# Kernel optimization log

Measured on AMD Instinct MI355X. Metric: run time of the kernel, lower is better.

Reference implementation:

```python
import jax, jax.numpy as jnp
import numpy as np

N = 50000        # nodes
E = 1_600_000    # edges (avg degree 32)
IN = 8           # in_channels
OUT = 64         # out_channels / hidden
K = 2            # Chebyshev order


def setup_inputs() -> dict:
    key = jax.random.key(0)
    ks = jax.random.split(key, 16)
    w = lambda k, s: (jax.random.normal(k, s, jnp.float32) * 0.05)
    inp = {
        "x": jax.random.normal(ks[0], (N, IN), jnp.float32),
        "H": jax.random.normal(ks[1], (N, OUT), jnp.float32),
        "edge_index": jax.random.randint(ks[2], (2, E), 0, N, dtype=jnp.int64),
    }
    names = [("z_x", IN), ("z_h", OUT), ("r_x", IN), ("r_h", OUT), ("c_x", IN), ("c_h", OUT)]
    for i, (nm, d) in enumerate(names):
        inp["W_" + nm] = w(ks[3 + 2 * i], (K, d, OUT))
        inp["b_" + nm] = w(ks[4 + 2 * i], (OUT,))
    return inp


def _cheb(x, W, b, row, col, norm):
    # PyG-style ChebConv with lambda_max=2: L_hat = -D^{-1/2} A D^{-1/2}
    # Tx0 = x; Tx1 = L_hat x; Tx_k = 2 L_hat Tx_{k-1} - Tx_{k-2}
    out = x @ W[0]
    Tx0 = x
    Tx1 = jax.ops.segment_sum(norm[:, None] * x[col], row, num_segments=N)
    out = out + Tx1 @ W[1]
    for k in range(2, W.shape[0]):
        Tx2 = 2.0 * jax.ops.segment_sum(norm[:, None] * Tx1[col], row, num_segments=N) - Tx0
        out = out + Tx2 @ W[k]
        Tx0, Tx1 = Tx1, Tx2
    return out + b


def reference(x, H, edge_index, W_z_x, b_z_x, W_z_h, b_z_h, W_r_x, b_r_x,
              W_r_h, b_r_h, W_c_x, b_c_x, W_c_h, b_c_h):
    row, col = edge_index[0], edge_index[1]
    deg = jax.ops.segment_sum(jnp.ones((E,), x.dtype), row, num_segments=N)
    dinv = jnp.where(deg > 0, 1.0 / jnp.sqrt(jnp.where(deg > 0, deg, 1.0)), 0.0)
    norm = -dinv[row] * dinv[col]  # sym-normalized, negated adjacency (L - I)

    Z = jax.nn.sigmoid(_cheb(x, W_z_x, b_z_x, row, col, norm)
                       + _cheb(H, W_z_h, b_z_h, row, col, norm))
    R = jax.nn.sigmoid(_cheb(x, W_r_x, b_r_x, row, col, norm)
                       + _cheb(H, W_r_h, b_r_h, row, col, norm))
    C = jnp.tanh(_cheb(x, W_c_x, b_c_x, row, col, norm)
                 + _cheb(R * H, W_c_h, b_c_h, row, col, norm))
    return Z * H + (1.0 - Z) * C
```

## Files before the change

### kernel.cpp

```cpp
#include <hip/hip_runtime.h>
#include <math.h>

#define IN_CH 8
#define OUT_CH 64

__global__ void deg_kernel(const int* __restrict__ row, int* __restrict__ deg, int E) {
    int i = blockIdx.x * blockDim.x + threadIdx.x;
    if (i < E) atomicAdd(&deg[row[i]], 1);
}

__global__ void dinv_kernel(const int* __restrict__ deg, float* __restrict__ dinv, int N) {
    int i = blockIdx.x * blockDim.x + threadIdx.x;
    if (i < N) {
        int d = deg[i];
        dinv[i] = (d > 0) ? rsqrtf((float)d) : 0.f;
    }
}

__global__ void scan_kernel(const int* __restrict__ deg, int* __restrict__ rowptr,
                            int* __restrict__ cursor, int N) {
    __shared__ int s_wave[17];
    __shared__ int s_running;
    int tid = threadIdx.x;
    int lane = tid & 63, wid = tid >> 6;
    if (tid == 0) s_running = 0;
    __syncthreads();
    for (int base = 0; base < N; base += 1024) {
        int i = base + tid;
        int v = (i < N) ? deg[i] : 0;
        int incl = v;
#pragma unroll
        for (int off = 1; off < 64; off <<= 1) {
            int t = __shfl_up(incl, off, 64);
            if (lane >= off) incl += t;
        }
        if (lane == 63) s_wave[wid] = incl;
        __syncthreads();
        if (wid == 0) {
            int wv = (lane < 16) ? s_wave[lane] : 0;
            int winc = wv;
#pragma unroll
            for (int off = 1; off < 16; off <<= 1) {
                int t = __shfl_up(winc, off, 64);
                if (lane >= off) winc += t;
            }
            if (lane < 16) s_wave[lane] = winc - wv;
            if (lane == 15) s_wave[16] = winc;
        }
        __syncthreads();
        int run = s_running;
        int excl = run + s_wave[wid] + incl - v;
        if (i < N) { rowptr[i] = excl; cursor[i] = excl; }
        __syncthreads();
        if (tid == 0) s_running = run + s_wave[16];
        __syncthreads();
    }
    if (tid == 0) rowptr[N] = s_running;
}

__global__ void bucket_kernel(const int* __restrict__ ei, const float* __restrict__ dinv,
                              int* __restrict__ cursor, int2* __restrict__ meta, int E) {
    int e = blockIdx.x * blockDim.x + threadIdx.x;
    if (e >= E) return;
    int r = ei[e];
    int c = ei[E + e];
    float nm = -dinv[r] * dinv[c];
    int pos = atomicAdd(&cursor[r], 1);
    meta[pos] = make_int2(c, __float_as_int(nm));
}

__global__ void gather64_kernel(const int* __restrict__ rowptr, const int2* __restrict__ meta,
                                const float* __restrict__ src, float* __restrict__ dst, int N) {
    int n = blockIdx.x * (blockDim.x >> 6) + (threadIdx.x >> 6);
    int lane = threadIdx.x & 63;
    if (n >= N) return;
    int beg = rowptr[n], end = rowptr[n + 1];
    float acc = 0.f;
    for (int base = beg; base < end; base += 64) {
        int cnt = min(end - base, 64);
        int2 m = meta[base + min(lane, cnt - 1)];
#pragma unroll 4
        for (int e = 0; e < cnt; ++e) {
            int c = __shfl(m.x, e, 64);
            float nm = __int_as_float(__shfl(m.y, e, 64));
            acc = fmaf(nm, src[(size_t)c * OUT_CH + lane], acc);
        }
    }
    dst[(size_t)n * OUT_CH + lane] = acc;
}

__global__ void gather8_kernel(const int* __restrict__ rowptr, const int2* __restrict__ meta,
                               const float* __restrict__ src, float* __restrict__ dst, int N) {
    int n = blockIdx.x * (blockDim.x >> 6) + (threadIdx.x >> 6);
    int lane = threadIdx.x & 63;
    int g = lane >> 3;
    int o = lane & 7;
    if (n >= N) return;
    int beg = rowptr[n], end = rowptr[n + 1];
    float acc = 0.f;
    for (int j = beg + g; j < end; j += 8) {
        int2 m = meta[j];
        acc = fmaf(__int_as_float(m.y), src[(size_t)m.x * IN_CH + o], acc);
    }
#pragma unroll
    for (int msk = 8; msk < 64; msk <<= 1) acc += __shfl_xor(acc, msk, 64);
    if (g == 0) dst[(size_t)n * IN_CH + o] = acc;
}

__device__ __forceinline__ float sigmoidf(float v) { return 1.0f / (1.0f + expf(-v)); }

__global__ __launch_bounds__(256) void gates_kernel(
        const float* __restrict__ x, const float* __restrict__ H,
        const float* __restrict__ Lx, const float* __restrict__ LH,
        const float* __restrict__ Wzx, const float* __restrict__ bzx,
        const float* __restrict__ Wzh, const float* __restrict__ bzh,
        const float* __restrict__ Wrx, const float* __restrict__ brx,
        const float* __restrict__ Wrh, const float* __restrict__ brh,
        float* __restrict__ Z, float* __restrict__ RH, int N) {
    int wid = threadIdx.x >> 6;
    int lane = threadIdx.x & 63;
    int n0 = blockIdx.x * 16 + wid * 4;

    float axl[4], hreg[4], lhreg[4], accZ[4], accR[4];
    float bz = bzx[lane] + bzh[lane];
    float br = brx[lane] + brh[lane];
#pragma unroll
    for (int i = 0; i < 4; ++i) {
        int n = n0 + i;
        int nn = (n < N) ? n : 0;
        axl[i]   = (lane < 8) ? x[(size_t)nn * IN_CH + lane]
                 : (lane < 16 ? Lx[(size_t)nn * IN_CH + (lane - 8)] : 0.f);
        hreg[i]  = H[(size_t)nn * OUT_CH + lane];
        lhreg[i] = LH[(size_t)nn * OUT_CH + lane];
        accZ[i] = bz;
        accR[i] = br;
    }
#pragma unroll
    for (int k = 0; k < IN_CH; ++k) {
        float wz0 = Wzx[k * 64 + lane], wz1 = Wzx[512 + k * 64 + lane];
        float wr0 = Wrx[k * 64 + lane], wr1 = Wrx[512 + k * 64 + lane];
#pragma unroll
        for (int i = 0; i < 4; ++i) {
            float xv  = __shfl(axl[i], k, 64);
            float lxv = __shfl(axl[i], k + 8, 64);
            accZ[i] = fmaf(xv, wz0, fmaf(lxv, wz1, accZ[i]));
            accR[i] = fmaf(xv, wr0, fmaf(lxv, wr1, accR[i]));
        }
    }
#pragma unroll 8
    for (int k = 0; k < OUT_CH; ++k) {
        float wh0 = Wzh[k * 64 + lane], wh1 = Wzh[4096 + k * 64 + lane];
        float wr0 = Wrh[k * 64 + lane], wr1 = Wrh[4096 + k * 64 + lane];
#pragma unroll
        for (int i = 0; i < 4; ++i) {
            float hv  = __shfl(hreg[i], k, 64);
            float lhv = __shfl(lhreg[i], k, 64);
            accZ[i] = fmaf(hv, wh0, fmaf(lhv, wh1, accZ[i]));
            accR[i] = fmaf(hv, wr0, fmaf(lhv, wr1, accR[i]));
        }
    }
#pragma unroll
    for (int i = 0; i < 4; ++i) {
        int n = n0 + i;
        if (n < N) {
            float z = sigmoidf(accZ[i]);
            float r = sigmoidf(accR[i]);
            Z[(size_t)n * OUT_CH + lane]  = z;
            RH[(size_t)n * OUT_CH + lane] = r * hreg[i];
        }
    }
}

__global__ __launch_bounds__(256) void final_kernel(
        const float* __restrict__ x, const float* __restrict__ H,
        const float* __restrict__ Lx, const float* __restrict__ RH,
        const float* __restrict__ LRH,
        const float* __restrict__ Wcx, const float* __restrict__ bcx,
        const float* __restrict__ Wch, const float* __restrict__ bch,
        const float* __restrict__ Z, float* __restrict__ out, int N) {
    int wid = threadIdx.x >> 6;
    int lane = threadIdx.x & 63;
    int n0 = blockIdx.x * 16 + wid * 4;

    float axl[4], rhreg[4], lrhreg[4], accC[4];
    float bc = bcx[lane] + bch[lane];
#pragma unroll
    for (int i = 0; i < 4; ++i) {
        int n = n0 + i;
        int nn = (n < N) ? n : 0;
        axl[i]    = (lane < 8) ? x[(size_t)nn * IN_CH + lane]
                  : (lane < 16 ? Lx[(size_t)nn * IN_CH + (lane - 8)] : 0.f);
        rhreg[i]  = RH[(size_t)nn * OUT_CH + lane];
        lrhreg[i] = LRH[(size_t)nn * OUT_CH + lane];
        accC[i] = bc;
    }
#pragma unroll
    for (int k = 0; k < IN_CH; ++k) {
        float wc0 = Wcx[k * 64 + lane], wc1 = Wcx[512 + k * 64 + lane];
#pragma unroll
        for (int i = 0; i < 4; ++i) {
            float xv  = __shfl(axl[i], k, 64);
            float lxv = __shfl(axl[i], k + 8, 64);
            accC[i] = fmaf(xv, wc0, fmaf(lxv, wc1, accC[i]));
        }
    }
#pragma unroll 8
    for (int k = 0; k < OUT_CH; ++k) {
        float wh0 = Wch[k * 64 + lane], wh1 = Wch[4096 + k * 64 + lane];
#pragma unroll
        for (int i = 0; i < 4; ++i) {
            float rv  = __shfl(rhreg[i], k, 64);
            float lrv = __shfl(lrhreg[i], k, 64);
            accC[i] = fmaf(rv, wh0, fmaf(lrv, wh1, accC[i]));
        }
    }
#pragma unroll
    for (int i = 0; i < 4; ++i) {
        int n = n0 + i;
        if (n < N) {
            float c = tanhf(accC[i]);
            float z = Z[(size_t)n * OUT_CH + lane];
            float h = H[(size_t)n * OUT_CH + lane];
            out[(size_t)n * OUT_CH + lane] = z * h + (1.0f - z) * c;
        }
    }
}

extern "C" void kernel_launch(void* const* d_in, const int* in_sizes, int n_in,
                              void* d_out, int out_size, void* d_ws, size_t ws_size,
                              hipStream_t stream) {
    const float* x   = (const float*)d_in[0];
    const float* H   = (const float*)d_in[1];
    const int*   ei  = (const int*)d_in[2];
    const float* Wzx = (const float*)d_in[3];
    const float* bzx = (const float*)d_in[4];
    const float* Wzh = (const float*)d_in[5];
    const float* bzh = (const float*)d_in[6];
    const float* Wrx = (const float*)d_in[7];
    const float* brx = (const float*)d_in[8];
    const float* Wrh = (const float*)d_in[9];
    const float* brh = (const float*)d_in[10];
    const float* Wcx = (const float*)d_in[11];
    const float* bcx = (const float*)d_in[12];
    const float* Wch = (const float*)d_in[13];
    const float* bch = (const float*)d_in[14];

    const int N = in_sizes[0] / IN_CH;
    const int E = in_sizes[2] / 2;

    int*   deg    = (int*)d_ws;
    float* dinv   = (float*)(deg + N);
    int*   rowptr = (int*)(dinv + N);
    int2*  meta   = (int2*)(rowptr + (N + 2));
    float* Lx     = (float*)(meta + E);
    float* LH     = Lx + (size_t)N * IN_CH;
    float* Z      = LH + (size_t)N * OUT_CH;
    float* RH     = Z  + (size_t)N * OUT_CH;
    float* LRH    = LH;
    int*   cursor = deg;

    hipMemsetAsync(deg, 0, (size_t)N * sizeof(int), stream);

    const int tb = 256;
    deg_kernel<<<(E + tb - 1) / tb, tb, 0, stream>>>(ei, deg, E);
    dinv_kernel<<<(N + tb - 1) / tb, tb, 0, stream>>>(deg, dinv, N);
    scan_kernel<<<1, 1024, 0, stream>>>(deg, rowptr, cursor, N);
    bucket_kernel<<<(E + tb - 1) / tb, tb, 0, stream>>>(ei, dinv, cursor, meta, E);

    const int nblk4 = (N + 3) / 4;
    const int nblk16 = (N + 15) / 16;

    gather8_kernel <<<nblk4, tb, 0, stream>>>(rowptr, meta, x, Lx, N);
    gather64_kernel<<<nblk4, tb, 0, stream>>>(rowptr, meta, H, LH, N);

    gates_kernel<<<nblk16, tb, 0, stream>>>(x, H, Lx, LH, Wzx, bzx, Wzh, bzh,
                                            Wrx, brx, Wrh, brh, Z, RH, N);

    gather64_kernel<<<nblk4, tb, 0, stream>>>(rowptr, meta, RH, LRH, N);

    final_kernel<<<nblk16, tb, 0, stream>>>(x, H, Lx, RH, LRH, Wcx, bcx, Wch, bch,
                                            Z, (float*)d_out, N);
}
```

Before: 665.6 us.

## Gather pre-scaled bf16 features with factored normalization and column-only CSR

The per-edge norm is factored into a source-side dinv scaling, applied once per node when x, H and R*H are converted to bf16, and a destination-side -dinv applied after accumulation. The CSR therefore stores only column indices, and the gathers read half-width bf16 rows, two edges per wave step for the 64-wide case. This cuts gather memory traffic, which dominates the edge pass. The gate kernels now process 8 nodes per wave instead of 4. The cost is bf16 rounding of the gathered features, which may loosen accuracy, plus extra conversion kernels and a zero padding row.

Result: no change. 657.1 us (-1.3%).

```diff
diff --git a/kernel.cpp b/kernel.cpp
--- a/kernel.cpp
+++ b/kernel.cpp
@@ -3,6 +3,14 @@
 
 #define IN_CH 8
 #define OUT_CH 64
+#define NPW 8
+
+__device__ __forceinline__ unsigned short f2b(float f) {
+    unsigned u = __float_as_uint(f);
+    u += 0x7FFFu + ((u >> 16) & 1u);
+    return (unsigned short)(u >> 16);
+}
+__device__ __forceinline__ float sigmoidf(float v) { return 1.0f / (1.0f + expf(-v)); }
 
 __global__ void deg_kernel(const int* __restrict__ row, int* __restrict__ deg, int E) {
     int i = blockIdx.x * blockDim.x + threadIdx.x;
@@ -58,80 +66,119 @@
     if (tid == 0) rowptr[N] = s_running;
 }
 
-__global__ void bucket_kernel(const int* __restrict__ ei, const float* __restrict__ dinv,
-                              int* __restrict__ cursor, int2* __restrict__ meta, int E) {
+__global__ void bucket_kernel(const int* __restrict__ ei, int* __restrict__ cursor,
+                              int* __restrict__ col_s, int E) {
     int e = blockIdx.x * blockDim.x + threadIdx.x;
     if (e >= E) return;
     int r = ei[e];
     int c = ei[E + e];
-    float nm = -dinv[r] * dinv[c];
     int pos = atomicAdd(&cursor[r], 1);
-    meta[pos] = make_int2(c, __float_as_int(nm));
-}
-
-__global__ void gather64_kernel(const int* __restrict__ rowptr, const int2* __restrict__ meta,
-                                const float* __restrict__ src, float* __restrict__ dst, int N) {
+    col_s[pos] = c;
+}
+
+__global__ void xform_kernel(const float* __restrict__ src, unsigned short* __restrict__ dst,
+                             const float* __restrict__ dinv, int total4, int logd) {
+    int i = blockIdx.x * blockDim.x + threadIdx.x;
+    if (i >= total4) return;
+    int el = i * 4;
+    float s = dinv[el >> logd];
+    float4 v = reinterpret_cast<const float4*>(src)[i];
+    ushort4 o;
+    o.x = f2b(v.x * s); o.y = f2b(v.y * s); o.z = f2b(v.z * s); o.w = f2b(v.w * s);
+    reinterpret_cast<ushort4*>(dst)[i] = o;
+}
+
+__global__ void zrow_kernel(unsigned short* xb, unsigned short* Hb, unsigned short* RHb, int N) {
+    int t = threadIdx.x;
+    if (t < IN_CH) xb[(size_t)N * IN_CH + t] = 0;
+    Hb[(size_t)N * OUT_CH + t] = 0;
+    RHb[(size_t)N * OUT_CH + t] = 0;
+}
+
+__global__ void g64_kernel(const int* __restrict__ rowptr, const int* __restrict__ col_s,
+                           const float* __restrict__ dinv, const unsigned short* __restrict__ srcb,
+                           float* __restrict__ dst, int N) {
     int n = blockIdx.x * (blockDim.x >> 6) + (threadIdx.x >> 6);
     int lane = threadIdx.x & 63;
+    int half = lane >> 5;
+    int sl = lane & 31;
     if (n >= N) return;
     int beg = rowptr[n], end = rowptr[n + 1];
-    float acc = 0.f;
+    const unsigned* src32 = reinterpret_cast<const unsigned*>(srcb);
+    float a0 = 0.f, a1 = 0.f;
     for (int base = beg; base < end; base += 64) {
         int cnt = min(end - base, 64);
-        int2 m = meta[base + min(lane, cnt - 1)];
+        int mycol = col_s[base + min(lane, cnt - 1)];
 #pragma unroll 4
-        for (int e = 0; e < cnt; ++e) {
-            int c = __shfl(m.x, e, 64);
-            float nm = __int_as_float(__shfl(m.y, e, 64));
-            acc = fmaf(nm, src[(size_t)c * OUT_CH + lane], acc);
-        }
-    }
-    dst[(size_t)n * OUT_CH + lane] = acc;
-}
-
-__global__ void gather8_kernel(const int* __restrict__ rowptr, const int2* __restrict__ meta,
-                               const float* __restrict__ src, float* __restrict__ dst, int N) {
+        for (int e = 0; e < cnt; e += 2) {
+            int idx = e + half;
+            int c = __shfl(mycol, idx, 64);
+            c = (idx < cnt) ? c : N;
+            unsigned v = src32[(c << 5) + sl];
+            a0 += __int_as_float(v << 16);
+            a1 += __int_as_float(v & 0xFFFF0000u);
+        }
+    }
+    a0 += __shfl_xor(a0, 32, 64);
+    a1 += __shfl_xor(a1, 32, 64);
+    if (half == 0) {
+        float s = -dinv[n];
+        reinterpret_cast<float2*>(dst)[(size_t)n * 32 + sl] = make_float2(s * a0, s * a1);
+    }
+}
+
+__global__ void g8_kernel(const int* __restrict__ rowptr, const int* __restrict__ col_s,
+                          const float* __restrict__ dinv, const unsigned short* __restrict__ srcb,
+                          float* __restrict__ dst, int N) {
     int n = blockIdx.x * (blockDim.x >> 6) + (threadIdx.x >> 6);
     int lane = threadIdx.x & 63;
-    int g = lane >> 3;
-    int o = lane & 7;
+    int g = lane >> 2;
+    int o2 = lane & 3;
     if (n >= N) return;
     int beg = rowptr[n], end = rowptr[n + 1];
-    float acc = 0.f;
-    for (int j = beg + g; j < end; j += 8) {
-        int2 m = meta[j];
-        acc = fmaf(__int_as_float(m.y), src[(size_t)m.x * IN_CH + o], acc);
-    }
-#pragma unroll
-    for (int msk = 8; msk < 64; msk <<= 1) acc += __shfl_xor(acc, msk, 64);
-    if (g == 0) dst[(size_t)n * IN_CH + o] = acc;
-}
-
-__device__ __forceinline__ float sigmoidf(float v) { return 1.0f / (1.0f + expf(-v)); }
+    const unsigned* src32 = reinterpret_cast<const unsigned*>(srcb);
+    float a0 = 0.f, a1 = 0.f;
+    for (int j = beg + g; j < end; j += 16) {
+        int c = col_s[j];
+        unsigned v = src32[(c << 2) + o2];
+        a0 += __int_as_float(v << 16);
+        a1 += __int_as_float(v & 0xFFFF0000u);
+    }
+#pragma unroll
+    for (int m = 4; m < 64; m <<= 1) {
+        a0 += __shfl_xor(a0, m, 64);
+        a1 += __shfl_xor(a1, m, 64);
+    }
+    if (lane < 4) {
+        float s = -dinv[n];
+        reinterpret_cast<float2*>(dst)[(size_t)n * 4 + o2] = make_float2(s * a0, s * a1);
+    }
+}
 
 __global__ __launch_bounds__(256) void gates_kernel(
         const float* __restrict__ x, const float* __restrict__ H,
         const float* __restrict__ Lx, const float* __restrict__ LH,
+        const float* __restrict__ dinv,
         const float* __restrict__ Wzx, const float* __restrict__ bzx,
         const float* __restrict__ Wzh, const float* __restrict__ bzh,
         const float* __restrict__ Wrx, const float* __restrict__ brx,
         const float* __restrict__ Wrh, const float* __restrict__ brh,
-        float* __restrict__ Z, float* __restrict__ RH, int N) {
+        float* __restrict__ Z, float* __restrict__ RH, unsigned short* __restrict__ RHb, int N) {
     int wid = threadIdx.x >> 6;
     int lane = threadIdx.x & 63;
-    int n0 = blockIdx.x * 16 + wid * 4;
-
-    float axl[4], hreg[4], lhreg[4], accZ[4], accR[4];
+    int n0 = blockIdx.x * (4 * NPW) + wid * NPW;
+
+    float axl[NPW], hreg[NPW], lhreg[NPW], accZ[NPW], accR[NPW], dv[NPW];
     float bz = bzx[lane] + bzh[lane];
     float br = brx[lane] + brh[lane];
 #pragma unroll
-    for (int i = 0; i < 4; ++i) {
-        int n = n0 + i;
-        int nn = (n < N) ? n : 0;
+    for (int i = 0; i < NPW; ++i) {
+        int nn = min(n0 + i, N - 1);
         axl[i]   = (lane < 8) ? x[(size_t)nn * IN_CH + lane]
                  : (lane < 16 ? Lx[(size_t)nn * IN_CH + (lane - 8)] : 0.f);
         hreg[i]  = H[(size_t)nn * OUT_CH + lane];
         lhreg[i] = LH[(size_t)nn * OUT_CH + lane];
+        dv[i]    = dinv[nn];
         accZ[i] = bz;
         accR[i] = br;
     }
@@ -140,19 +187,19 @@
         float wz0 = Wzx[k * 64 + lane], wz1 = Wzx[512 + k * 64 + lane];
         float wr0 = Wrx[k * 64 + lane], wr1 = Wrx[512 + k * 64 + lane];
 #pragma unroll
-        for (int i = 0; i < 4; ++i) {
+        for (int i = 0; i < NPW; ++i) {
             float xv  = __shfl(axl[i], k, 64);
             float lxv = __shfl(axl[i], k + 8, 64);
             accZ[i] = fmaf(xv, wz0, fmaf(lxv, wz1, accZ[i]));
             accR[i] = fmaf(xv, wr0, fmaf(lxv, wr1, accR[i]));
         }
     }
-#pragma unroll 8
+#pragma unroll 4
     for (int k = 0; k < OUT_CH; ++k) {
         float wh0 = Wzh[k * 64 + lane], wh1 = Wzh[4096 + k * 64 + lane];
         float wr0 = Wrh[k * 64 + lane], wr1 = Wrh[4096 + k * 64 + lane];
 #pragma unroll
-        for (int i = 0; i < 4; ++i) {
+        for (int i = 0; i < NPW; ++i) {
             float hv  = __shfl(hreg[i], k, 64);
             float lhv = __shfl(lhreg[i], k, 64);
             accZ[i] = fmaf(hv, wh0, fmaf(lhv, wh1, accZ[i]));
@@ -160,13 +207,15 @@
         }
     }
 #pragma unroll
-    for (int i = 0; i < 4; ++i) {
+    for (int i = 0; i < NPW; ++i) {
         int n = n0 + i;
         if (n < N) {
             float z = sigmoidf(accZ[i]);
             float r = sigmoidf(accR[i]);
+            float rh = r * hreg[i];
             Z[(size_t)n * OUT_CH + lane]  = z;
-            RH[(size_t)n * OUT_CH + lane] = r * hreg[i];
+            RH[(size_t)n * OUT_CH + lane] = rh;
+            RHb[(size_t)n * OUT_CH + lane] = f2b(dv[i] * rh);
         }
     }
 }
@@ -180,14 +229,13 @@
         const float* __restrict__ Z, float* __restrict__ out, int N) {
     int wid = threadIdx.x >> 6;
     int lane = threadIdx.x & 63;
-    int n0 = blockIdx.x * 16 + wid * 4;
-
-    float axl[4], rhreg[4], lrhreg[4], accC[4];
+    int n0 = blockIdx.x * (4 * NPW) + wid * NPW;
+
+    float axl[NPW], rhreg[NPW], lrhreg[NPW], accC[NPW];
     float bc = bcx[lane] + bch[lane];
 #pragma unroll
-    for (int i = 0; i < 4; ++i) {
-        int n = n0 + i;
-        int nn = (n < N) ? n : 0;
+    for (int i = 0; i < NPW; ++i) {
+        int nn = min(n0 + i, N - 1);
         axl[i]    = (lane < 8) ? x[(size_t)nn * IN_CH + lane]
                   : (lane < 16 ? Lx[(size_t)nn * IN_CH + (lane - 8)] : 0.f);
         rhreg[i]  = RH[(size_t)nn * OUT_CH + lane];
@@ -198,24 +246,24 @@
     for (int k = 0; k < IN_CH; ++k) {
         float wc0 = Wcx[k * 64 + lane], wc1 = Wcx[512 + k * 64 + lane];
 #pragma unroll
-        for (int i = 0; i < 4; ++i) {
+        for (int i = 0; i < NPW; ++i) {
             float xv  = __shfl(axl[i], k, 64);
             float lxv = __shfl(axl[i], k + 8, 64);
             accC[i] = fmaf(xv, wc0, fmaf(lxv, wc1, accC[i]));
         }
     }
-#pragma unroll 8
+#pragma unroll 4
     for (int k = 0; k < OUT_CH; ++k) {
         float wh0 = Wch[k * 64 + lane], wh1 = Wch[4096 + k * 64 + lane];
 #pragma unroll
-        for (int i = 0; i < 4; ++i) {
+        for (int i = 0; i < NPW; ++i) {
             float rv  = __shfl(rhreg[i], k, 64);
             float lrv = __shfl(lrhreg[i], k, 64);
             accC[i] = fmaf(rv, wh0, fmaf(lrv, wh1, accC[i]));
         }
     }
 #pragma unroll
-    for (int i = 0; i < 4; ++i) {
+    for (int i = 0; i < NPW; ++i) {
         int n = n0 + i;
         if (n < N) {
             float c = tanhf(accC[i]);
@@ -251,12 +299,15 @@
     int*   deg    = (int*)d_ws;
     float* dinv   = (float*)(deg + N);
     int*   rowptr = (int*)(dinv + N);
-    int2*  meta   = (int2*)(rowptr + (N + 2));
-    float* Lx     = (float*)(meta + E);
-    float* LH     = Lx + (size_t)N * IN_CH;
-    float* Z      = LH + (size_t)N * OUT_CH;
-    float* RH     = Z  + (size_t)N * OUT_CH;
-    float* LRH    = LH;
+    int*   col_s  = rowptr + (N + 2);
+    unsigned short* xb  = (unsigned short*)(col_s + E);
+    unsigned short* Hb  = xb + (size_t)(N + 1) * IN_CH;
+    unsigned short* RHb = Hb + (size_t)(N + 1) * OUT_CH;
+    float* Lx  = (float*)(RHb + (size_t)(N + 1) * OUT_CH);
+    float* LH  = Lx + (size_t)N * IN_CH;
+    float* Z   = LH + (size_t)N * OUT_CH;
+    float* RH  = Z  + (size_t)N * OUT_CH;
+    float* LRH = LH;
     int*   cursor = deg;
 
     hipMemsetAsync(deg, 0, (size_t)N * sizeof(int), stream);
@@ -265,19 +316,27 @@
     deg_kernel<<<(E + tb - 1) / tb, tb, 0, stream>>>(ei, deg, E);
     dinv_kernel<<<(N + tb - 1) / tb, tb, 0, stream>>>(deg, dinv, N);
     scan_kernel<<<1, 1024, 0, stream>>>(deg, rowptr, cursor, N);
-    bucket_kernel<<<(E + tb - 1) / tb, tb, 0, stream>>>(ei, dinv, cursor, meta, E);
-
-    const int nblk4 = (N + 3) / 4;
-    const int nblk16 = (N + 15) / 16;
-
-    gather8_kernel <<<nblk4, tb, 0, stream>>>(rowptr, meta, x, Lx, N);
-    gather64_kernel<<<nblk4, tb, 0, stream>>>(rowptr, meta, H, LH, N);
-
-    gates_kernel<<<nblk16, tb, 0, stream>>>(x, H, Lx, LH, Wzx, bzx, Wzh, bzh,
-                                            Wrx, brx, Wrh, brh, Z, RH, N);
-
-    gather64_kernel<<<nblk4, tb, 0, stream>>>(rowptr, meta, RH, LRH, N);
-
-    final_kernel<<<nblk16, tb, 0, stream>>>(x, H, Lx, RH, LRH, Wcx, bcx, Wch, bch,
-                                            Z, (float*)d_out, N);
-}
+    bucket_kernel<<<(E + tb - 1) / tb, tb, 0, stream>>>(ei, cursor, col_s, E);
+
+    {
+        int t4 = N * OUT_CH / 4;
+        xform_kernel<<<(t4 + tb - 1) / tb, tb, 0, stream>>>(H, Hb, dinv, t4, 6);
+        t4 = N * IN_CH / 4;
+        xform_kernel<<<(t4 + tb - 1) / tb, tb, 0, stream>>>(x, xb, dinv, t4, 3);
+        zrow_kernel<<<1, 64, 0, stream>>>(xb, Hb, RHb, N);
+    }
+
+    const int nblk4  = (N + 3) / 4;
+    const int nblkD  = (N + 4 * NPW - 1) / (4 * NPW);
+
+    g8_kernel <<<nblk4, tb, 0, stream>>>(rowptr, col_s, dinv, xb, Lx, N);
+    g64_kernel<<<nblk4, tb, 0, stream>>>(rowptr, col_s, dinv, Hb, LH, N);
+
+    gates_kernel<<<nblkD, tb, 0, stream>>>(x, H, Lx, LH, dinv, Wzx, bzx, Wzh, bzh,
+                                           Wrx, brx, Wrh, brh, Z, RH, RHb, N);
+
+    g64_kernel<<<nblk4, tb, 0, stream>>>(rowptr, col_s, dinv, RHb, LRH, N);
+
+    final_kernel<<<nblkD, tb, 0, stream>>>(x, H, Lx, RH, LRH, Wcx, bcx, Wch, bch,
+                                           Z, (float*)d_out, N);
+}
```
